# Optimization experiments

Hardware: AMD Instinct MI355X
Metric: run time of the kernel (lower is better)

## Reference

```python
import jax, jax.numpy as jnp
import numpy as np

D = 256      # d_model
SUB = 3      # number of adjacency subsets
GROUPS = 8
N, T, V = 32, 256, 19


def setup_inputs() -> dict:
    key = jax.random.key(0)
    ks = jax.random.split(key, 4)
    return {
        "x": jax.random.normal(ks[0], (N, T, V, D), jnp.float32),
        "para": jax.random.normal(ks[1], (3, GROUPS, V, V), jnp.float32),
        "linear_weight": jax.random.normal(ks[2], (D, D * SUB), jnp.float32) * 0.05,
        "linear_bias": jax.random.normal(ks[3], (1, D * SUB, 1, 1), jnp.float32) * 0.05,
        "bn_gamma": jnp.ones((D * SUB,), jnp.float32),
        "bn_beta": jnp.zeros((D * SUB,), jnp.float32),
        "bn1_gamma": jnp.ones((D,), jnp.float32),
        "bn1_beta": jnp.zeros((D,), jnp.float32),
    }


def _bn(x, gamma, beta, eps=1e-5):
    # BatchNorm2d (training mode): stats over (n, t, v) per channel
    m = jnp.mean(x, axis=(0, 2, 3), keepdims=True)
    v = jnp.var(x, axis=(0, 2, 3), keepdims=True)
    return (x - m) * jax.lax.rsqrt(v + eps) * gamma[None, :, None, None] + beta[None, :, None, None]


def reference(x, para, linear_weight, linear_bias, bn_gamma, bn_beta, bn1_gamma, bn1_beta):
    xc = jnp.transpose(x, (0, 3, 1, 2))                 # (n, c, t, v)
    # expand per-group adjacency to per-channel: (3, D, V, V)
    A = jnp.tile(para, (1, D // GROUPS, 1, 1))
    # L2 row-normalize along last dim (matches torch.norm(dim=-1))
    A = A / (jnp.linalg.norm(A, axis=-1, keepdims=True) + 1e-4)
    # channel mixing: (n, 3c, t, v)
    y = jnp.einsum('nctw,cd->ndtw', xc, linear_weight)
    y = _bn(y + linear_bias, bn_gamma, bn_beta)
    n, kc, t, v = y.shape
    y = y.reshape(n, SUB, kc // SUB, t, v)              # (n, k, c, t, v)
    # per-channel tiny 19x19 adjacency matmul
    y = jnp.einsum('nkctv,kcvw->nctw', y, A)            # (n, c, t, v)
    out = jax.nn.relu(_bn(y + xc, bn1_gamma, bn1_beta))
    return jnp.transpose(out, (0, 2, 3, 1))             # (n, t, v, c)
```

## Files before the change

### kernel.cpp

```cpp
#include <hip/hip_runtime.h>

typedef unsigned short u16;
typedef unsigned int u32;
typedef float f32x4 __attribute__((ext_vector_type(4)));
typedef __bf16 bf16x8 __attribute__((ext_vector_type(8)));

#define M_ALL 155648.0f
#define GP 168

__device__ __forceinline__ u16 f2bf(float f) {
  union { float f; u32 u; } x; x.f = f;
  u32 u = x.u;
  u += 0x7FFFu + ((u >> 16) & 1u);
  return (u16)(u >> 16);
}
__device__ __forceinline__ float bf2f(u16 h) {
  union { u32 u; float f; } x; x.u = ((u32)h) << 16;
  return x.f;
}
__device__ __forceinline__ f32x4 zero4() { f32x4 z = {0.f, 0.f, 0.f, 0.f}; return z; }

__device__ __forceinline__ int xs_idx(int m, int c) {
  return m * 256 + ((((c >> 3) ^ (m & 7)) << 3) | (c & 7));
}
__device__ __forceinline__ int y2_idx(int r, int kvp) {
  int sw = (r & 7) ^ ((r >> 3) & 7);
  return r * 64 + ((((kvp >> 3) ^ sw) << 3) | (kvp & 7));
}

__global__ void k_prep(const float* __restrict__ para, u16* __restrict__ wa2) {
  __shared__ float aL[3 * 8 * 19 * 19];
  int tid = threadIdx.x;
  if (tid < 456) {
    int k = tid / 152, rem = tid % 152, g = rem / 19, v = rem % 19;
    int base = ((k * 8 + g) * 19 + v) * 19;
    float ss = 0.f;
    #pragma unroll
    for (int w = 0; w < 19; ++w) { float a = para[base + w]; ss += a * a; }
    float inv = 1.f / (sqrtf(ss) + 1e-4f);
    #pragma unroll
    for (int w = 0; w < 19; ++w) aL[base + w] = para[base + w] * inv;
  }
  __syncthreads();
  for (int i = tid; i < 8 * 20 * 64; i += 512) {
    int g = i / 1280, rem = i % 1280, w = rem >> 6, kvp = rem & 63;
    u16 val = 0;
    if (w < 19 && kvp < 57) {
      int k = kvp / 19, v = kvp - 19 * k;
      val = f2bf(aL[((k * 8 + g) * 19 + v) * 19 + w]);
    }
    wa2[i] = val;
  }
}

__global__ void k_wt(const float* __restrict__ W, u16* __restrict__ wt) {
  int idx = blockIdx.x * 512 + threadIdx.x;
  int d = idx >> 8, c = idx & 255;
  wt[idx] = f2bf(W[c * 768 + d]);
}

__global__ __launch_bounds__(256) void k_tr(const float* __restrict__ x,
                                            u16* __restrict__ xbf,
                                            u16* __restrict__ xTt,
                                            float* __restrict__ colsum) {
  __shared__ u16 tl[64 * 258];
  __shared__ float csA[1024];
  int t = threadIdx.x;
  int l = t & 63, w = t >> 6;
  float s0 = 0.f, s1 = 0.f, s2 = 0.f, s3 = 0.f;
  const float4* x4 = reinterpret_cast<const float4*>(x);

  for (int tt = 0; tt < 4; ++tt) {
    int m0 = (blockIdx.x * 4 + tt) * 64;
    __syncthreads();
    #pragma unroll 4
    for (int it = 0; it < 16; ++it) {
      int ml = it * 4 + w;
      int m = m0 + ml;
      float4 f = x4[(size_t)m * 64 + l];
      u16 b0 = f2bf(f.x), b1 = f2bf(f.y), b2 = f2bf(f.z), b3 = f2bf(f.w);
      s0 += f.x; s1 += f.y; s2 += f.z; s3 += f.w;
      ushort4 pk; pk.x = b0; pk.y = b1; pk.z = b2; pk.w = b3;
      *reinterpret_cast<ushort4*>(&xbf[(size_t)m * 256 + 4 * l]) = pk;
      u32 lo = (u32)b0 | ((u32)b1 << 16);
      u32 hi = (u32)b2 | ((u32)b3 << 16);
      *reinterpret_cast<u32*>(&tl[ml * 258 + 4 * l]) = lo;
      *reinterpret_cast<u32*>(&tl[ml * 258 + 4 * l + 2]) = hi;
    }
    __syncthreads();
    int k = l >> 3, g = l & 7;
    #pragma unroll
    for (int p = 0; p < 8; ++p) {
      int c = p * 32 + w * 8 + k;
      union { u16 v[8]; bf16x8 v8; } uv;
      #pragma unroll
      for (int j = 0; j < 8; ++j) uv.v[j] = tl[(8 * g + j) * 258 + c];
      int mg = m0 + 8 * g;
      int b = mg / 608;
      int mm = mg - b * 608;
      *reinterpret_cast<bf16x8*>(&xTt[((size_t)b * 256 + c) * 608 + mm]) = uv.v8;
    }
  }
  csA[w * 256 + 4 * l + 0] = s0;
  csA[w * 256 + 4 * l + 1] = s1;
  csA[w * 256 + 4 * l + 2] = s2;
  csA[w * 256 + 4 * l + 3] = s3;
  __syncthreads();
  float s = csA[t] + csA[256 + t] + csA[512 + t] + csA[768 + t];
  atomicAdd(&colsum[t], s);
}

template<int BF>
__global__ __launch_bounds__(512, 2) void k_gram(const float* __restrict__ x,
                                                 const u16* __restrict__ xTt,
                                                 float* __restrict__ Gp,
                                                 float* __restrict__ colsum) {
  __shared__ u16 xsT[256 * GP];
  __shared__ float scs[512];
  int tid = threadIdx.x, bid = blockIdx.x;
  int c = tid & 255, mh = tid >> 8;
  int lane = tid & 63, wave = tid >> 6;
  int cl = lane & 15, q = lane >> 4;

  if (tid < 256) {
    *reinterpret_cast<uint2*>(&xsT[tid * GP + 152]) = make_uint2(0u, 0u);
    *reinterpret_cast<uint2*>(&xsT[tid * GP + 156]) = make_uint2(0u, 0u);
  }

  float cs = 0.f;
  f32x4 acc[2][16];
  #pragma unroll
  for (int ri = 0; ri < 2; ++ri)
    #pragma unroll
    for (int j = 0; j < 16; ++j) acc[ri][j] = zero4();

  for (int ss = 0; ss < 4; ++ss) {
    int sl = bid * 4 + ss;
    __syncthreads();
    if constexpr (BF) {
      const u16* xc = xTt + (size_t)bid * 155648;
      #pragma unroll 1
      for (int i = tid; i < 4864; i += 512) {
        int cc = i / 19, g = i - cc * 19;
        *reinterpret_cast<bf16x8*>(&xsT[cc * GP + g * 8]) =
            *reinterpret_cast<const bf16x8*>(&xc[cc * 608 + ss * 152 + g * 8]);
      }
    } else {
      const float* xb = x + (size_t)sl * 152 * 256;
      #pragma unroll 1
      for (int it = 0; it < 19; ++it) {
        int m0 = it * 8 + mh * 4;
        float v0 = xb[(m0 + 0) * 256 + c];
        float v1 = xb[(m0 + 1) * 256 + c];
        float v2 = xb[(m0 + 2) * 256 + c];
        float v3 = xb[(m0 + 3) * 256 + c];
        cs += v0 + v1 + v2 + v3;
        uint2 p;
        p.x = (u32)f2bf(v0) | ((u32)f2bf(v1) << 16);
        p.y = (u32)f2bf(v2) | ((u32)f2bf(v3) << 16);
        *reinterpret_cast<uint2*>(&xsT[c * GP + m0]) = p;
      }
    }
    __syncthreads();
    #pragma unroll
    for (int s = 0; s < 5; ++s) {
      int kof = s * 32 + q * 8;
      bf16x8 a0 = *reinterpret_cast<const bf16x8*>(&xsT[(wave * 16 + cl) * GP + kof]);
      bf16x8 a1 = *reinterpret_cast<const bf16x8*>(&xsT[((wave + 8) * 16 + cl) * GP + kof]);
      #pragma unroll
      for (int ct2 = 0; ct2 < 16; ++ct2) {
        bf16x8 b = *reinterpret_cast<const bf16x8*>(&xsT[(ct2 * 16 + cl) * GP + kof]);
        acc[0][ct2] = __builtin_amdgcn_mfma_f32_16x16x32_bf16(a0, b, acc[0][ct2], 0, 0, 0);
        acc[1][ct2] = __builtin_amdgcn_mfma_f32_16x16x32_bf16(a1, b, acc[1][ct2], 0, 0, 0);
      }
    }
  }
  #pragma unroll
  for (int ri = 0; ri < 2; ++ri) {
    int ct = wave + ri * 8;
    int tb = 16 * ct - (ct * (ct - 1)) / 2 - ct;
    #pragma unroll
    for (int ct2 = 0; ct2 < 16; ++ct2) {
      if (ct2 >= ct) {
        float* dst = Gp + ((size_t)(tb + ct2) * 256 + bid) * 256;
        #pragma unroll
        for (int r4 = 0; r4 < 4; ++r4)
          dst[(q * 4 + r4) * 16 + cl] = acc[ri][ct2][r4];
      }
    }
  }
  if constexpr (!BF) {
    scs[tid] = cs;
    __syncthreads();
    if (tid < 256) atomicAdd(&colsum[tid], scs[tid] + scs[tid + 256]);
  }
}

__global__ __launch_bounds__(256) void k_red(const float* __restrict__ Gp,
                                             float* __restrict__ G) {
  int b = blockIdx.x;
  int e = threadIdx.x;
  int ct = 0;
  #pragma unroll
  for (int t = 1; t < 16; ++t)
    if (b >= 16 * t - (t * (t - 1)) / 2) ct = t;
  int ct2 = ct + (b - (16 * ct - (ct * (ct - 1)) / 2));
  const float* src = Gp + (size_t)b * 65536;
  float s = 0.f;
  #pragma unroll 8
  for (int p = 0; p < 256; ++p) s += src[p * 256 + e];
  int row = e >> 4, col = e & 15;
  int rr = ct * 16 + row, cc = ct2 * 16 + col;
  G[rr * 256 + cc] = s;
  G[cc * 256 + rr] = s;
}

__global__ __launch_bounds__(256) void k_f1(const float* __restrict__ G,
                                            const float* __restrict__ colsum,
                                            const float* __restrict__ W,
                                            const float* __restrict__ gam,
                                            const float* __restrict__ bet,
                                            float* __restrict__ ST) {
  __shared__ float wd[256];
  __shared__ float red[16];
  int d = blockIdx.x, c = threadIdx.x;
  float wv = W[c * 768 + d];
  wd[c] = wv;
  __syncthreads();
  float dot = 0.f;
  const float* Gr = G + c * 256;
  #pragma unroll 4
  for (int j = 0; j < 256; ++j) dot += Gr[j] * wd[j];
  float part = wv * dot;
  float mpart = colsum[c] * wv;
  #pragma unroll
  for (int o = 32; o; o >>= 1) { part += __shfl_down(part, o); mpart += __shfl_down(mpart, o); }
  int lane = c & 63, w = c >> 6;
  if (lane == 0) { red[w] = part; red[8 + w] = mpart; }
  __syncthreads();
  if (c == 0) {
    float qv = red[0] + red[1] + red[2] + red[3];
    float ms = red[8] + red[9] + red[10] + red[11];
    float mean = ms / M_ALL;
    float var = qv / M_ALL - mean * mean;
    float S = gam[d] * rsqrtf(var + 1e-5f);
    ST[d] = S;
    ST[768 + d] = bet[d] - mean * S;
  }
}

template<int BF>
__global__ __launch_bounds__(512, 2) void k_main(const float* __restrict__ x,
                                                 const u16* __restrict__ xbf,
                                                 const u16* __restrict__ wt,
                                                 const u16* __restrict__ wa2,
                                                 const float* __restrict__ ST,
                                                 float* __restrict__ sumz,
                                                 float* __restrict__ out) {
  __shared__ u16 xs[152 * 256];
  __shared__ u16 y2[512 * 64];
  __shared__ float scrz[1024];
  int tid = threadIdx.x;
  int bid = blockIdx.x;
  size_t obase = (size_t)bid * 152 * 256;

  if constexpr (BF) {
    const u16* xb16 = xbf + (size_t)bid * 152 * 256;
    int w = tid >> 6, lane = tid & 63;
    int ch = lane & 31, half = lane >> 5;
    for (int it = 0; it < 10; ++it) {
      int m = it * 16 + 2 * w + half;
      if (m < 152) {
        const u16* src = xb16 + m * 256 + ((ch ^ (m & 7)) << 3);
        *reinterpret_cast<bf16x8*>(&xs[m * 256 + (ch << 3)]) =
            *reinterpret_cast<const bf16x8*>(src);
      }
    }
  } else {
    const float* xbase = x + (size_t)bid * 152 * 256;
    int r = tid >> 6, c4 = (tid & 63) << 2;
    for (int it = 0; it < 19; ++it) {
      int m = it * 8 + r;
      float4 f = *reinterpret_cast<const float4*>(xbase + m * 256 + c4);
      uint2 p;
      p.x = (u32)f2bf(f.x) | ((u32)f2bf(f.y) << 16);
      p.y = (u32)f2bf(f.z) | ((u32)f2bf(f.w) << 16);
      *reinterpret_cast<uint2*>(&xs[xs_idx(m, c4)]) = p;
    }
  }

  int lane = tid & 63, wave = tid >> 6;
  int mhalf = wave & 1, nt3 = wave >> 1;
  int cl = lane & 15, q = lane >> 4;
  int g = wave;
  const bf16x8* wtv = reinterpret_cast<const bf16x8*>(wt);
  float* zbufF = reinterpret_cast<float*>(y2);

  bf16x8 bfr[2][2];
  #pragma unroll
  for (int ks = 0; ks < 2; ++ks)
    #pragma unroll
    for (int nt = 0; nt < 2; ++nt) {
      int w = nt * 16 + cl; int wc = (w < 20) ? w : 19;
      bfr[ks][nt] = *reinterpret_cast<const bf16x8*>(&wa2[(g * 20 + wc) * 64 + ks * 32 + q * 8]);
    }

  int arow[5], mlow[5];
  #pragma unroll
  for (int i = 0; i < 5; ++i) {
    int rr = mhalf * 80 + i * 16 + cl;
    if (rr > 151) rr = 151;
    arow[i] = rr * 256; mlow[i] = rr & 7;
  }
  __syncthreads();

  for (int nc = 0; nc < 4; ++nc) {
    f32x4 acc[5][3];
    #pragma unroll
    for (int i = 0; i < 5; ++i)
      #pragma unroll
      for (int jj = 0; jj < 3; ++jj) acc[i][jj] = zero4();
    for (int s = 0; s < 8; ++s) {
      int sq4 = s * 4 + q;
      bf16x8 b[3];
      #pragma unroll
      for (int jj = 0; jj < 3; ++jj) {
        int j = nt3 * 3 + jj;
        int d = (j >> 2) * 256 + nc * 64 + (j & 3) * 16 + cl;
        b[jj] = wtv[d * 32 + sq4];
      }
      #pragma unroll
      for (int i = 0; i < 5; ++i) {
        bf16x8 a = *reinterpret_cast<const bf16x8*>(&xs[arow[i] + ((sq4 ^ mlow[i]) << 3)]);
        #pragma unroll
        for (int jj = 0; jj < 3; ++jj)
          acc[i][jj] = __builtin_amdgcn_mfma_f32_16x16x32_bf16(a, b[jj], acc[i][jj], 0, 0, 0);
      }
    }
    __syncthreads();

    #pragma unroll
    for (int kk = 0; kk < 7; ++kk)
      y2[y2_idx(tid, 57 + kk)] = 0;

    #pragma unroll
    for (int jj = 0; jj < 3; ++jj) {
      int j = nt3 * 3 + jj;
      int ksub = j >> 2;
      int c_local = (j & 3) * 16 + cl;
      int d = ksub * 256 + nc * 64 + c_local;
      float Sc = ST[d], Tc = ST[768 + d];
      #pragma unroll
      for (int i = 0; i < 5; ++i) {
        int mb = mhalf * 80 + i * 16 + q * 4;
        #pragma unroll
        for (int r4 = 0; r4 < 4; ++r4) {
          int m = mb + r4;
          if (m < 152) {
            int t = (m * 27) >> 9;
            int v = m - t * 19;
            int kvp = ksub * 19 + v;
            int r = t * 64 + c_local;
            y2[y2_idx(r, kvp)] = f2bf(acc[i][jj][r4] * Sc + Tc);
          }
        }
      }
    }
    __syncthreads();

    f32x4 zacc[4][2];
    #pragma unroll
    for (int mt = 0; mt < 4; ++mt) { zacc[mt][0] = zero4(); zacc[mt][1] = zero4(); }
    #pragma unroll
    for (int ks = 0; ks < 2; ++ks) {
      #pragma unroll
      for (int mt = 0; mt < 4; ++mt) {
        int tc = mt * 16 + cl;
        int t = tc >> 3, c8 = tc & 7;
        int r = t * 64 + c8 * 8 + g;
        int ch = (ks * 4 + q) ^ g ^ c8;
        bf16x8 afr = *reinterpret_cast<const bf16x8*>(&y2[r * 64 + (ch << 3)]);
        #pragma unroll
        for (int nt = 0; nt < 2; ++nt)
          zacc[mt][nt] = __builtin_amdgcn_mfma_f32_16x16x32_bf16(afr, bfr[ks][nt], zacc[mt][nt], 0, 0, 0);
      }
    }
    __syncthreads();

    #pragma unroll
    for (int mt = 0; mt < 4; ++mt)
      #pragma unroll
      for (int nt = 0; nt < 2; ++nt) {
        int w = nt * 16 + cl;
        if (w < 19) {
          #pragma unroll
          for (int r4 = 0; r4 < 4; ++r4) {
            int mm = mt * 16 + q * 4 + r4;
            int t = mm >> 3, c8 = mm & 7;
            zbufF[(c8 * 8 + g) * 153 + t * 19 + w] = zacc[mt][nt][r4];
          }
        }
      }
    __syncthreads();

    float sz = 0.f, sq = 0.f;
    int cloc = tid & 63;
    int cglob = nc * 64 + cloc;
    #pragma unroll 1
    for (int rep = 0; rep < 19; ++rep) {
      int mp = rep * 8 + (tid >> 6);
      float z = zbufF[cloc * 153 + mp] + bf2f(xs[xs_idx(mp, cglob)]);
      out[obase + (size_t)mp * 256 + cglob] = z;
      sz += z; sq += z * z;
    }
    scrz[(tid >> 6) * 64 + cloc] = sz;
    scrz[512 + (tid >> 6) * 64 + cloc] = sq;
    __syncthreads();
    if (tid < 128) {
      int comp = tid >> 6, c = tid & 63;
      float v = 0.f;
      #pragma unroll
      for (int h = 0; h < 8; ++h) v += scrz[comp * 512 + h * 64 + c];
      atomicAdd(&sumz[comp * 256 + nc * 64 + c], v);
    }
  }
}

__global__ void k_f2(const float* __restrict__ statz, const float* __restrict__ gam,
                     const float* __restrict__ bet, float* __restrict__ S1T1) {
  int c = threadIdx.x;
  float inv = 1.f / M_ALL;
  float mz = statz[c] * inv;
  float qv = statz[256 + c] * inv;
  float var = qv - mz * mz;
  float Sc = gam[c] * rsqrtf(var + 1e-5f);
  S1T1[c] = Sc;
  S1T1[256 + c] = bet[c] - mz * Sc;
}

__global__ __launch_bounds__(256) void k_relu(float* __restrict__ out,
                                              const float* __restrict__ S1T1) {
  int tid = threadIdx.x;
  int lane = tid & 63;
  int wv = ((blockIdx.x << 8) + tid) >> 6;
  const float4* s14 = reinterpret_cast<const float4*>(S1T1);
  float4 sv = s14[lane], tv = s14[64 + lane];
  float4* o4 = reinterpret_cast<float4*>(out);
  #pragma unroll 1
  for (int r = 0; r < 19; ++r) {
    size_t i = ((size_t)r * 8192 + wv) * 64 + lane;
    float4 f = o4[i];
    f.x = fmaxf(f.x * sv.x + tv.x, 0.f);
    f.y = fmaxf(f.y * sv.y + tv.y, 0.f);
    f.z = fmaxf(f.z * sv.z + tv.z, 0.f);
    f.w = fmaxf(f.w * sv.w + tv.w, 0.f);
    o4[i] = f;
  }
}

extern "C" void kernel_launch(void* const* d_in, const int* in_sizes, int n_in,
                              void* d_out, int out_size, void* d_ws, size_t ws_size,
                              hipStream_t stream) {
  const float* x    = (const float*)d_in[0];
  const float* para = (const float*)d_in[1];
  const float* W    = (const float*)d_in[2];
  const float* bng  = (const float*)d_in[4];
  const float* bnb  = (const float*)d_in[5];
  const float* bn1g = (const float*)d_in[6];
  const float* bn1b = (const float*)d_in[7];
  float* out = (float*)d_out;

  char* ws = (char*)d_ws;
  u16* wt     = (u16*)ws;
  u16* wa2    = (u16*)(ws + 393216);
  float* G    = (float*)(ws + 413696);
  float* csum = (float*)(ws + 675840);
  float* sumz = (float*)(ws + 676864);
  float* ST   = (float*)(ws + 678912);
  float* S1T1 = (float*)(ws + 685056);
  u16* xbf    = (u16*)(ws + 687104);
  u16* xTt  = (u16*)d_out;
  float* Gp = (float*)((char*)d_out + 79691776);

  const size_t NEED = 687104u + 79691776u;

  hipMemsetAsync(ws + 675840, 0, 1024 + 2048, stream);
  k_prep<<<dim3(1),    dim3(512), 0, stream>>>(para, wa2);
  k_wt  <<<dim3(384),  dim3(512), 0, stream>>>(W, wt);
  if (ws_size >= NEED) {
    k_tr  <<<dim3(608),  dim3(256), 0, stream>>>(x, xbf, xTt, csum);
    k_gram<1><<<dim3(256),  dim3(512), 0, stream>>>(x, xTt, Gp, csum);
    k_red <<<dim3(136),  dim3(256), 0, stream>>>(Gp, G);
    k_f1  <<<dim3(768),  dim3(256), 0, stream>>>(G, csum, W, bng, bnb, ST);
    k_main<1><<<dim3(1024), dim3(512), 0, stream>>>(x, xbf, wt, wa2, ST, sumz, out);
  } else {
    float* Gp0 = (float*)d_out;
    k_gram<0><<<dim3(256),  dim3(512), 0, stream>>>(x, nullptr, Gp0, csum);
    k_red <<<dim3(136),  dim3(256), 0, stream>>>(Gp0, G);
    k_f1  <<<dim3(768),  dim3(256), 0, stream>>>(G, csum, W, bng, bnb, ST);
    k_main<0><<<dim3(1024), dim3(512), 0, stream>>>(x, nullptr, wt, wa2, ST, sumz, out);
  }
  k_f2  <<<dim3(1),    dim3(256), 0, stream>>>(sumz, bn1g, bn1b, S1T1);
  k_relu<<<dim3(2048), dim3(256), 0, stream>>>(out, S1T1);
}
```

Baseline: 657.2 us.

## Fuse transpose/bf16 conversion with Gram MFMA and split reduction across blocks

New measurement: 607.5 us. 7.6% less time.

```diff
diff --git a/kernel.cpp b/kernel.cpp
--- a/kernel.cpp
+++ b/kernel.cpp
@@ -59,23 +59,32 @@
   wt[idx] = f2bf(W[c * 768 + d]);
 }
 
-__global__ __launch_bounds__(256) void k_tr(const float* __restrict__ x,
-                                            u16* __restrict__ xbf,
-                                            u16* __restrict__ xTt,
-                                            float* __restrict__ colsum) {
+__global__ __launch_bounds__(512, 2) void k_trg(const float* __restrict__ x,
+                                                u16* __restrict__ xbf,
+                                                float* __restrict__ Gp,
+                                                float* __restrict__ colsum) {
   __shared__ u16 tl[64 * 258];
-  __shared__ float csA[1024];
-  int t = threadIdx.x;
-  int l = t & 63, w = t >> 6;
+  __shared__ u16 tlT[256 * 72];
+  __shared__ float csA[2048];
+  int tid = threadIdx.x, bid = blockIdx.x;
+  int l = tid & 63, w = tid >> 6;
+  int cl = l & 15, q = l >> 4;
+  int kk = l >> 3, g = l & 7;
+
   float s0 = 0.f, s1 = 0.f, s2 = 0.f, s3 = 0.f;
+  f32x4 acc[2][16];
+  #pragma unroll
+  for (int ri = 0; ri < 2; ++ri)
+    #pragma unroll
+    for (int j = 0; j < 16; ++j) acc[ri][j] = zero4();
+
   const float4* x4 = reinterpret_cast<const float4*>(x);
-
   for (int tt = 0; tt < 4; ++tt) {
-    int m0 = (blockIdx.x * 4 + tt) * 64;
-    __syncthreads();
-    #pragma unroll 4
-    for (int it = 0; it < 16; ++it) {
-      int ml = it * 4 + w;
+    int m0 = bid * 256 + tt * 64;
+    __syncthreads();
+    #pragma unroll
+    for (int r = 0; r < 8; ++r) {
+      int ml = r * 8 + w;
       int m = m0 + ml;
       float4 f = x4[(size_t)m * 64 + l];
       u16 b0 = f2bf(f.x), b1 = f2bf(f.y), b2 = f2bf(f.z), b3 = f2bf(f.w);
@@ -88,17 +97,43 @@
       *reinterpret_cast<u32*>(&tl[ml * 258 + 4 * l + 2]) = hi;
     }
     __syncthreads();
-    int k = l >> 3, g = l & 7;
-    #pragma unroll
-    for (int p = 0; p < 8; ++p) {
-      int c = p * 32 + w * 8 + k;
+    #pragma unroll
+    for (int p = 0; p < 4; ++p) {
+      int c = p * 64 + w * 8 + kk;
       union { u16 v[8]; bf16x8 v8; } uv;
       #pragma unroll
       for (int j = 0; j < 8; ++j) uv.v[j] = tl[(8 * g + j) * 258 + c];
-      int mg = m0 + 8 * g;
-      int b = mg / 608;
-      int mm = mg - b * 608;
-      *reinterpret_cast<bf16x8*>(&xTt[((size_t)b * 256 + c) * 608 + mm]) = uv.v8;
+      *reinterpret_cast<bf16x8*>(&tlT[c * 72 + 8 * (g ^ (c & 7))]) = uv.v8;
+    }
+    __syncthreads();
+    #pragma unroll
+    for (int s = 0; s < 2; ++s) {
+      int ch = s * 4 + q;
+      int ca0 = w * 16 + cl;
+      int ca1 = (w + 8) * 16 + cl;
+      bf16x8 a0 = *reinterpret_cast<const bf16x8*>(&tlT[ca0 * 72 + 8 * (ch ^ (ca0 & 7))]);
+      bf16x8 a1 = *reinterpret_cast<const bf16x8*>(&tlT[ca1 * 72 + 8 * (ch ^ (ca1 & 7))]);
+      #pragma unroll
+      for (int ct2 = 0; ct2 < 16; ++ct2) {
+        int cb = ct2 * 16 + cl;
+        bf16x8 b = *reinterpret_cast<const bf16x8*>(&tlT[cb * 72 + 8 * (ch ^ (cb & 7))]);
+        acc[0][ct2] = __builtin_amdgcn_mfma_f32_16x16x32_bf16(a0, b, acc[0][ct2], 0, 0, 0);
+        acc[1][ct2] = __builtin_amdgcn_mfma_f32_16x16x32_bf16(a1, b, acc[1][ct2], 0, 0, 0);
+      }
+    }
+  }
+  #pragma unroll
+  for (int ri = 0; ri < 2; ++ri) {
+    int ct = w + ri * 8;
+    int tb = 16 * ct - (ct * (ct - 1)) / 2 - ct;
+    #pragma unroll
+    for (int ct2 = 0; ct2 < 16; ++ct2) {
+      if (ct2 >= ct) {
+        float* dst = Gp + ((size_t)(tb + ct2) * 608 + bid) * 256;
+        #pragma unroll
+        for (int r4 = 0; r4 < 4; ++r4)
+          dst[(q * 4 + r4) * 16 + cl] = acc[ri][ct2][r4];
+      }
     }
   }
   csA[w * 256 + 4 * l + 0] = s0;
@@ -106,15 +141,17 @@
   csA[w * 256 + 4 * l + 2] = s2;
   csA[w * 256 + 4 * l + 3] = s3;
   __syncthreads();
-  float s = csA[t] + csA[256 + t] + csA[512 + t] + csA[768 + t];
-  atomicAdd(&colsum[t], s);
-}
-
-template<int BF>
-__global__ __launch_bounds__(512, 2) void k_gram(const float* __restrict__ x,
-                                                 const u16* __restrict__ xTt,
-                                                 float* __restrict__ Gp,
-                                                 float* __restrict__ colsum) {
+  if (tid < 256) {
+    float s = 0.f;
+    #pragma unroll
+    for (int h = 0; h < 8; ++h) s += csA[h * 256 + tid];
+    atomicAdd(&colsum[tid], s);
+  }
+}
+
+__global__ __launch_bounds__(512, 2) void k_gram0(const float* __restrict__ x,
+                                                  float* __restrict__ Gp,
+                                                  float* __restrict__ colsum) {
   __shared__ u16 xsT[256 * GP];
   __shared__ float scs[512];
   int tid = threadIdx.x, bid = blockIdx.x;
@@ -136,30 +173,20 @@
 
   for (int ss = 0; ss < 4; ++ss) {
     int sl = bid * 4 + ss;
-    __syncthreads();
-    if constexpr (BF) {
-      const u16* xc = xTt + (size_t)bid * 155648;
-      #pragma unroll 1
-      for (int i = tid; i < 4864; i += 512) {
-        int cc = i / 19, g = i - cc * 19;
-        *reinterpret_cast<bf16x8*>(&xsT[cc * GP + g * 8]) =
-            *reinterpret_cast<const bf16x8*>(&xc[cc * 608 + ss * 152 + g * 8]);
-      }
-    } else {
-      const float* xb = x + (size_t)sl * 152 * 256;
-      #pragma unroll 1
-      for (int it = 0; it < 19; ++it) {
-        int m0 = it * 8 + mh * 4;
-        float v0 = xb[(m0 + 0) * 256 + c];
-        float v1 = xb[(m0 + 1) * 256 + c];
-        float v2 = xb[(m0 + 2) * 256 + c];
-        float v3 = xb[(m0 + 3) * 256 + c];
-        cs += v0 + v1 + v2 + v3;
-        uint2 p;
-        p.x = (u32)f2bf(v0) | ((u32)f2bf(v1) << 16);
-        p.y = (u32)f2bf(v2) | ((u32)f2bf(v3) << 16);
-        *reinterpret_cast<uint2*>(&xsT[c * GP + m0]) = p;
-      }
+    const float* xb = x + (size_t)sl * 152 * 256;
+    __syncthreads();
+    #pragma unroll 1
+    for (int it = 0; it < 19; ++it) {
+      int m0 = it * 8 + mh * 4;
+      float v0 = xb[(m0 + 0) * 256 + c];
+      float v1 = xb[(m0 + 1) * 256 + c];
+      float v2 = xb[(m0 + 2) * 256 + c];
+      float v3 = xb[(m0 + 3) * 256 + c];
+      cs += v0 + v1 + v2 + v3;
+      uint2 p;
+      p.x = (u32)f2bf(v0) | ((u32)f2bf(v1) << 16);
+      p.y = (u32)f2bf(v2) | ((u32)f2bf(v3) << 16);
+      *reinterpret_cast<uint2*>(&xsT[c * GP + m0]) = p;
     }
     __syncthreads();
     #pragma unroll
@@ -189,30 +216,30 @@
       }
     }
   }
-  if constexpr (!BF) {
-    scs[tid] = cs;
-    __syncthreads();
-    if (tid < 256) atomicAdd(&colsum[tid], scs[tid] + scs[tid + 256]);
-  }
+  scs[tid] = cs;
+  __syncthreads();
+  if (tid < 256) atomicAdd(&colsum[tid], scs[tid] + scs[tid + 256]);
 }
 
 __global__ __launch_bounds__(256) void k_red(const float* __restrict__ Gp,
-                                             float* __restrict__ G) {
-  int b = blockIdx.x;
+                                             float* __restrict__ G, int npart) {
+  int bx = blockIdx.x;
+  int b = bx >> 2, h = bx & 3;
   int e = threadIdx.x;
   int ct = 0;
   #pragma unroll
   for (int t = 1; t < 16; ++t)
     if (b >= 16 * t - (t * (t - 1)) / 2) ct = t;
   int ct2 = ct + (b - (16 * ct - (ct * (ct - 1)) / 2));
-  const float* src = Gp + (size_t)b * 65536;
+  const float* src = Gp + (size_t)b * npart * 256;
+  int pl = npart >> 2;
   float s = 0.f;
   #pragma unroll 8
-  for (int p = 0; p < 256; ++p) s += src[p * 256 + e];
+  for (int i = 0; i < pl; ++i) s += src[(size_t)(h * pl + i) * 256 + e];
   int row = e >> 4, col = e & 15;
   int rr = ct * 16 + row, cc = ct2 * 16 + col;
-  G[rr * 256 + cc] = s;
-  G[cc * 256 + rr] = s;
+  atomicAdd(&G[rr * 256 + cc], s);
+  if (ct != ct2) atomicAdd(&G[cc * 256 + rr], s);
 }
 
 __global__ __launch_bounds__(256) void k_f1(const float* __restrict__ G,
@@ -479,24 +506,21 @@
   float* ST   = (float*)(ws + 678912);
   float* S1T1 = (float*)(ws + 685056);
   u16* xbf    = (u16*)(ws + 687104);
-  u16* xTt  = (u16*)d_out;
-  float* Gp = (float*)((char*)d_out + 79691776);
+  float* Gp = (float*)d_out;
 
   const size_t NEED = 687104u + 79691776u;
 
-  hipMemsetAsync(ws + 675840, 0, 1024 + 2048, stream);
+  hipMemsetAsync(ws + 413696, 0, 262144 + 1024 + 2048, stream);
   k_prep<<<dim3(1),    dim3(512), 0, stream>>>(para, wa2);
   k_wt  <<<dim3(384),  dim3(512), 0, stream>>>(W, wt);
   if (ws_size >= NEED) {
-    k_tr  <<<dim3(608),  dim3(256), 0, stream>>>(x, xbf, xTt, csum);
-    k_gram<1><<<dim3(256),  dim3(512), 0, stream>>>(x, xTt, Gp, csum);
-    k_red <<<dim3(136),  dim3(256), 0, stream>>>(Gp, G);
+    k_trg <<<dim3(608),  dim3(512), 0, stream>>>(x, xbf, Gp, csum);
+    k_red <<<dim3(544),  dim3(256), 0, stream>>>(Gp, G, 608);
     k_f1  <<<dim3(768),  dim3(256), 0, stream>>>(G, csum, W, bng, bnb, ST);
     k_main<1><<<dim3(1024), dim3(512), 0, stream>>>(x, xbf, wt, wa2, ST, sumz, out);
   } else {
-    float* Gp0 = (float*)d_out;
-    k_gram<0><<<dim3(256),  dim3(512), 0, stream>>>(x, nullptr, Gp0, csum);
-    k_red <<<dim3(136),  dim3(256), 0, stream>>>(Gp0, G);
+    k_gram0<<<dim3(256), dim3(512), 0, stream>>>(x, Gp, csum);
+    k_red <<<dim3(544),  dim3(256), 0, stream>>>(Gp, G, 256);
     k_f1  <<<dim3(768),  dim3(256), 0, stream>>>(G, csum, W, bng, bnb, ST);
     k_main<0><<<dim3(1024), dim3(512), 0, stream>>>(x, nullptr, wt, wa2, ST, sumz, out);
   }
```
